# Kernel tuning notes

Hardware: AMD Instinct MI355X
Metric: run time of the kernel (lower is better)

The kernel has to match this reference:

```python
import jax, jax.numpy as jnp
import numpy as np

N_NODES = 50000


def setup_inputs() -> dict:
    key = jax.random.key(0)
    ks = jax.random.split(key, 16)
    f = lambda k, shape: jax.random.normal(k, shape, dtype=jnp.float32) * 0.05
    ri = lambda k, shape: jax.random.randint(k, shape, 0, N_NODES, dtype=jnp.int32)
    return {
        "x": jax.random.normal(ks[0], (N_NODES, 128), dtype=jnp.float32),
        "W1": f(ks[1], (4, 128, 128)),
        "b1": f(ks[2], (4, 128)),
        "W2": f(ks[3], (4, 128, 128)),
        "b2": f(ks[4], (4, 128)),
        "P1w": f(ks[5], (128, 128)),
        "P1b": f(ks[6], (128,)),
        "P2w": f(ks[7], (128, 2)),
        "P2b": f(ks[8], (2,)),
        "src": ri(ks[9], (4, 200000)),
        "dst": ri(ks[10], (4, 200000)),
        "pos_src": ri(ks[11], (4, 200000)),
        "pos_dst": ri(ks[12], (4, 200000)),
        "neg_src": ri(ks[13], (4, 200000)),
        "neg_dst": ri(ks[14], (4, 200000)),
    }


def _hetero_conv(h, src, dst, W, b):
    """One HeteroGraphConv layer: per-relation GraphConv(norm='right'), no activation.

    h: [N, F_in]; src/dst: [R, E]; W: [R, F_in, F_out]; b: [R, F_out].
    Returns per-relation outputs [R, N, F_out] (caller applies activation then sums).
    """
    # sum of source features into destination nodes, per relation
    agg = jax.vmap(lambda s, d: jax.ops.segment_sum(h[s], d, num_segments=N_NODES))(src, dst)  # [R,N,Fin]
    deg = jax.vmap(lambda d: jax.ops.segment_sum(jnp.ones(d.shape, jnp.float32), d, num_segments=N_NODES))(dst)  # [R,N]
    norm = jnp.where(deg > 0, 1.0 / jnp.maximum(deg, 1.0), 0.0)[..., None]  # norm='right': 1/in_degree
    return jnp.einsum("rnf,rfo->rno", agg * norm, W) + b[:, None, :]


def _edge_scores(h, e_src, e_dst, P1w, P1b, P2w, P2b):
    # h[src]*h[dst] -> Linear -> ReLU -> Linear -> softmax -> class-1 prob
    e = h[e_src] * h[e_dst]  # [R,E,F]
    z = jax.nn.relu(jnp.einsum("ref,fo->reo", e, P1w) + P1b)
    logits = jnp.einsum("reo,oc->rec", z, P2w) + P2b
    return jax.nn.softmax(logits, axis=-1)[..., 1]  # [R,E]


def reference(x, W1, b1, W2, b2, P1w, P1b, P2w, P2b,
              src, dst, pos_src, pos_dst, neg_src, neg_dst):
    # Layer 1: relu per relation conv, then HeteroGraphConv sum across relations
    h = jnp.sum(jax.nn.relu(_hetero_conv(x, src, dst, W1, b1)), axis=0)  # [N, hidden]
    # Layer 2: no activation, sum across relations
    h = jnp.sum(_hetero_conv(h, src, dst, W2, b2), axis=0)  # [N, out]
    pos = _edge_scores(h, pos_src, pos_dst, P1w, P1b, P2w, P2b)
    neg = _edge_scores(h, neg_src, neg_dst, P1w, P1b, P2w, P2b)
    return (pos, neg)
```

## Files before the change

kernel.cpp:

```cpp
#include <hip/hip_runtime.h>
#include <hip/hip_bf16.h>
#include <math.h>

#define N_NODES 50000
#define N_EDGES 200000
#define N_REL   4
#define FDIM    128
#define SCAN_BLKS 49

typedef __attribute__((ext_vector_type(8))) short short8;
typedef __attribute__((ext_vector_type(4))) float f32x4;

static __device__ __forceinline__ ushort f2bf(float f) {
  union { float f; unsigned u; } v; v.f = f;
  unsigned r = v.u + 0x7fff + ((v.u >> 16) & 1);
  return (ushort)(r >> 16);
}
static __device__ __forceinline__ unsigned pk2(float lo, float hi) {
  __hip_bfloat162 t = __float22bfloat162_rn(make_float2(lo, hi));
  union { __hip_bfloat162 b; unsigned u; } v; v.b = t;
  return v.u;
}
static __device__ __forceinline__ float lo2f(unsigned u) {
  union { unsigned u; float f; } v; v.u = u << 16; return v.f;
}
static __device__ __forceinline__ float hi2f(unsigned u) {
  union { unsigned u; float f; } v; v.u = u & 0xffff0000u; return v.f;
}

__global__ void cnt_kernel(const int* __restrict__ dst, int* __restrict__ cnt) {
  int i = blockIdx.x * 256 + threadIdx.x;
  if (i < N_REL * N_EDGES) {
    int r = i / N_EDGES;
    atomicAdd(&cnt[r * N_NODES + dst[i]], 1);
  }
}

__global__ __launch_bounds__(1024) void scanA_kernel(
    const int* __restrict__ cnt, int* __restrict__ rowp,
    float* __restrict__ nrm, int* __restrict__ bsum) {
  int r = blockIdx.y, bx = blockIdx.x, t = threadIdx.x;
  int n = bx * 1024 + t;
  int g = r * N_NODES + n;
  int c = 0;
  if (n < N_NODES) {
    c = cnt[g];
    nrm[g] = c > 0 ? 1.f / (float)c : 0.f;
  }
  __shared__ int ts[1024];
  ts[t] = c;
  __syncthreads();
  for (int off = 1; off < 1024; off <<= 1) {
    int v = 0;
    if (t >= off) v = ts[t - off];
    __syncthreads();
    ts[t] += v;
    __syncthreads();
  }
  if (n < N_NODES) rowp[g] = ts[t] - c;
  if (t == 1023) bsum[r * SCAN_BLKS + bx] = ts[t];
}

__global__ void scanB_kernel(int* __restrict__ bsum) {
  int r = threadIdx.x;
  if (r < N_REL) {
    int run = r * N_EDGES;
    for (int b = 0; b < SCAN_BLKS; ++b) {
      int t = bsum[r * SCAN_BLKS + b];
      bsum[r * SCAN_BLKS + b] = run;
      run += t;
    }
  }
}

__global__ void scanC_kernel(int* __restrict__ rowp, int* __restrict__ cursor,
                             const int* __restrict__ bsum) {
  int i = blockIdx.x * 256 + threadIdx.x;
  if (i < N_REL * N_NODES) {
    int r = i / N_NODES;
    int n = i - r * N_NODES;
    int v = rowp[i] + bsum[r * SCAN_BLKS + (n >> 10)];
    rowp[i] = v;
    cursor[i] = v;
  }
}

__global__ void fill_kernel(const int* __restrict__ src, const int* __restrict__ dst,
                            int* __restrict__ cursor, int* __restrict__ csr_s) {
  int i = blockIdx.x * 256 + threadIdx.x;
  if (i < N_REL * N_EDGES) {
    int r = i / N_EDGES;
    int pos = atomicAdd(&cursor[r * N_NODES + dst[i]], 1);
    csr_s[pos] = src[i];
  }
}

__global__ void prep_all_kernel(const float* __restrict__ x, ushort* __restrict__ xb,
                                const float* __restrict__ P1w, ushort* __restrict__ bT,
                                const float* __restrict__ W1, ushort* __restrict__ wT1,
                                const float* __restrict__ W2, ushort* __restrict__ wT2) {
  const int NC = N_NODES * FDIM / 4;
  int i = blockIdx.x * 256 + threadIdx.x;
  if (i < NC) {
    float4 v = ((const float4*)x)[i];
    ((uint2*)xb)[i] = make_uint2(pk2(v.x, v.y), pk2(v.z, v.w));
    return;
  }
  int i2 = i - NC;
  if (i2 < FDIM * FDIM) {
    int c = i2 >> 7, k = i2 & 127;
    bT[i2] = f2bf(P1w[k * FDIM + c]);
    return;
  }
  i2 -= FDIM * FDIM;
  if (i2 < N_REL * FDIM * FDIM) {
    int r = i2 >> 14, c = (i2 >> 7) & 127, k = i2 & 127;
    wT1[i2] = f2bf(W1[(r << 14) + (k << 7) + c]);
    return;
  }
  i2 -= N_REL * FDIM * FDIM;
  if (i2 < N_REL * FDIM * FDIM) {
    int r = i2 >> 14, c = (i2 >> 7) & 127, k = i2 & 127;
    wT2[i2] = f2bf(W2[(r << 14) + (k << 7) + c]);
  }
}

__global__ __launch_bounds__(256) void conv_part_kernel(
    const ushort* __restrict__ hin, const int* __restrict__ rowp,
    const int* __restrict__ cnt, const float* __restrict__ nrm,
    const int* __restrict__ csr_s, const ushort* __restrict__ wT,
    const float* __restrict__ bias, ushort* __restrict__ hpart, int do_relu) {
  __shared__ __align__(16) short elds[64 * 128];
  __shared__ float nrm_lds[64];
  int tid  = threadIdx.x;
  int wave = tid >> 6, lane = tid & 63;
  int base = blockIdx.x * 64;
  int r    = blockIdx.y;
  int ig = tid >> 4, l16 = tid & 15;

  if (tid < 64) {
    int n = base + tid;
    nrm_lds[tid] = (n < N_NODES) ? nrm[r * N_NODES + n] : 0.f;
  }

  for (int rr = ig; rr < 64; rr += 16) {
    int n = base + rr;
    float a8[8];
#pragma unroll
    for (int q = 0; q < 8; ++q) a8[q] = 0.f;
    if (n < N_NODES) {
      int idx = r * N_NODES + n;
      int beg = rowp[idx], num = cnt[idx];
      int j = 0;
      for (; j + 4 <= num; j += 4) {
        int s0 = csr_s[beg + j], s1 = csr_s[beg + j + 1];
        int s2 = csr_s[beg + j + 2], s3 = csr_s[beg + j + 3];
        uint4 v0 = *(const uint4*)(hin + (size_t)s0 * FDIM + l16 * 8);
        uint4 v1 = *(const uint4*)(hin + (size_t)s1 * FDIM + l16 * 8);
        uint4 v2 = *(const uint4*)(hin + (size_t)s2 * FDIM + l16 * 8);
        uint4 v3 = *(const uint4*)(hin + (size_t)s3 * FDIM + l16 * 8);
        a8[0] += lo2f(v0.x) + lo2f(v1.x) + lo2f(v2.x) + lo2f(v3.x);
        a8[1] += hi2f(v0.x) + hi2f(v1.x) + hi2f(v2.x) + hi2f(v3.x);
        a8[2] += lo2f(v0.y) + lo2f(v1.y) + lo2f(v2.y) + lo2f(v3.y);
        a8[3] += hi2f(v0.y) + hi2f(v1.y) + hi2f(v2.y) + hi2f(v3.y);
        a8[4] += lo2f(v0.z) + lo2f(v1.z) + lo2f(v2.z) + lo2f(v3.z);
        a8[5] += hi2f(v0.z) + hi2f(v1.z) + hi2f(v2.z) + hi2f(v3.z);
        a8[6] += lo2f(v0.w) + lo2f(v1.w) + lo2f(v2.w) + lo2f(v3.w);
        a8[7] += hi2f(v0.w) + hi2f(v1.w) + hi2f(v2.w) + hi2f(v3.w);
      }
      for (; j < num; ++j) {
        int s = csr_s[beg + j];
        uint4 v = *(const uint4*)(hin + (size_t)s * FDIM + l16 * 8);
        a8[0] += lo2f(v.x); a8[1] += hi2f(v.x);
        a8[2] += lo2f(v.y); a8[3] += hi2f(v.y);
        a8[4] += lo2f(v.z); a8[5] += hi2f(v.z);
        a8[6] += lo2f(v.w); a8[7] += hi2f(v.w);
      }
    }
    int byte = rr * 256 + l16 * 16;
    byte ^= (rr & 7) << 4;
    *(uint4*)((char*)elds + byte) =
        make_uint4(pk2(a8[0], a8[1]), pk2(a8[2], a8[3]),
                   pk2(a8[4], a8[5]), pk2(a8[6], a8[7]));
  }
  __syncthreads();

  short8 bfrag[2][4];
#pragma unroll
  for (int t2 = 0; t2 < 2; ++t2) {
    int c = wave * 32 + t2 * 16 + (lane & 15);
#pragma unroll
    for (int k0 = 0; k0 < 4; ++k0)
      bfrag[t2][k0] = *(const short8*)(wT + ((size_t)r * FDIM + c) * FDIM + k0 * 32 + (lane >> 4) * 8);
  }

  ushort* hp = hpart + (size_t)r * N_NODES * FDIM;
#pragma unroll
  for (int tr = 0; tr < 4; ++tr) {
    int arow = tr * 16 + (lane & 15);
    short8 afrag[4];
#pragma unroll
    for (int k0 = 0; k0 < 4; ++k0) {
      int byte = arow * 256 + k0 * 64 + (lane >> 4) * 16;
      byte ^= (arow & 7) << 4;
      afrag[k0] = *(const short8*)((const char*)elds + byte);
    }
#pragma unroll
    for (int t2 = 0; t2 < 2; ++t2) {
      f32x4 acc = {0.f, 0.f, 0.f, 0.f};
#pragma unroll
      for (int k0 = 0; k0 < 4; ++k0)
        acc = __builtin_amdgcn_mfma_f32_16x16x32_bf16(afrag[k0], bfrag[t2][k0], acc, 0, 0, 0);
      int col = wave * 32 + t2 * 16 + (lane & 15);
      float bv = bias[r * FDIM + col];
#pragma unroll
      for (int j2 = 0; j2 < 4; ++j2) {
        int n = base + tr * 16 + (lane >> 4) * 4 + j2;
        if (n < N_NODES) {
          float nr = nrm_lds[tr * 16 + (lane >> 4) * 4 + j2];
          float v = acc[j2] * nr + bv;
          if (do_relu) v = fmaxf(v, 0.f);
          hp[(size_t)n * FDIM + col] = f2bf(v);
        }
      }
    }
  }
}

__global__ void finalize_kernel(const ushort* __restrict__ hpart, ushort* __restrict__ hout) {
  int i = blockIdx.x * 256 + threadIdx.x;
  const int NV = N_NODES * FDIM / 8;
  if (i < NV) {
    uint4 a = ((const uint4*)hpart)[i];
    uint4 b = ((const uint4*)(hpart + (size_t)N_NODES * FDIM))[i];
    uint4 c = ((const uint4*)(hpart + (size_t)2 * N_NODES * FDIM))[i];
    uint4 d = ((const uint4*)(hpart + (size_t)3 * N_NODES * FDIM))[i];
    float s0 = lo2f(a.x) + lo2f(b.x) + lo2f(c.x) + lo2f(d.x);
    float s1 = hi2f(a.x) + hi2f(b.x) + hi2f(c.x) + hi2f(d.x);
    float s2 = lo2f(a.y) + lo2f(b.y) + lo2f(c.y) + lo2f(d.y);
    float s3 = hi2f(a.y) + hi2f(b.y) + hi2f(c.y) + hi2f(d.y);
    float s4 = lo2f(a.z) + lo2f(b.z) + lo2f(c.z) + lo2f(d.z);
    float s5 = hi2f(a.z) + hi2f(b.z) + hi2f(c.z) + hi2f(d.z);
    float s6 = lo2f(a.w) + lo2f(b.w) + lo2f(c.w) + lo2f(d.w);
    float s7 = hi2f(a.w) + hi2f(b.w) + hi2f(c.w) + hi2f(d.w);
    ((uint4*)hout)[i] = make_uint4(pk2(s0, s1), pk2(s2, s3), pk2(s4, s5), pk2(s6, s7));
  }
}

__global__ __launch_bounds__(256) void edge_mfma_kernel(
    const ushort* __restrict__ hb,
    const int* __restrict__ psrc, const int* __restrict__ pdst,
    const int* __restrict__ nsrc, const int* __restrict__ ndst,
    const ushort* __restrict__ bT, const float* __restrict__ P1b,
    const float* __restrict__ P2w, const float* __restrict__ P2b,
    float* __restrict__ out) {
  __shared__ __align__(16) short elds[64 * 128];
  __shared__ float partials[4][64];

  int tid  = threadIdx.x;
  int wave = tid >> 6, lane = tid & 63;
  int b = blockIdx.x;
  const int *esrc, *edst;
  float* o;
  int base;
  if (b < (N_REL * N_EDGES) / 64) {
    esrc = psrc; edst = pdst; o = out; base = b * 64;
  } else {
    esrc = nsrc; edst = ndst; o = out + (size_t)N_REL * N_EDGES;
    base = (b - (N_REL * N_EDGES) / 64) * 64;
  }

  int c0 = (2 * wave) * 16 + (lane & 15);
  int c1 = c0 + 16;
  float bz0 = P1b[c0], bz1 = P1b[c1];
  float wd0 = P2w[c0 * 2 + 1] - P2w[c0 * 2];
  float wd1 = P2w[c1 * 2 + 1] - P2w[c1 * 2];
  float cdiff = P2b[1] - P2b[0];

  short8 bfrag[2][4];
#pragma unroll
  for (int t2 = 0; t2 < 2; ++t2) {
    int c = (2 * wave + t2) * 16 + (lane & 15);
#pragma unroll
    for (int k0 = 0; k0 < 4; ++k0)
      bfrag[t2][k0] = *(const short8*)(bT + (size_t)c * 128 + k0 * 32 + (lane >> 4) * 8);
  }

  uint4 av[4], gv[4];
#pragma unroll
  for (int j = 0; j < 4; ++j) {
    int flat = j * 256 + tid;
    int row = flat >> 4, f8 = flat & 15;
    int ge = base + row;
    int s = esrc[ge], d = edst[ge];
    av[j] = *(const uint4*)(hb + (size_t)s * FDIM + f8 * 8);
    gv[j] = *(const uint4*)(hb + (size_t)d * FDIM + f8 * 8);
  }
#pragma unroll
  for (int j = 0; j < 4; ++j) {
    int flat = j * 256 + tid;
    int row = flat >> 4, f8 = flat & 15;
    unsigned w0 = pk2(lo2f(av[j].x) * lo2f(gv[j].x), hi2f(av[j].x) * hi2f(gv[j].x));
    unsigned w1 = pk2(lo2f(av[j].y) * lo2f(gv[j].y), hi2f(av[j].y) * hi2f(gv[j].y));
    unsigned w2 = pk2(lo2f(av[j].z) * lo2f(gv[j].z), hi2f(av[j].z) * hi2f(gv[j].z));
    unsigned w3 = pk2(lo2f(av[j].w) * lo2f(gv[j].w), hi2f(av[j].w) * hi2f(gv[j].w));
    int byte = row * 256 + f8 * 16;
    byte ^= (row & 7) << 4;
    *(uint4*)((char*)elds + byte) = make_uint4(w0, w1, w2, w3);
  }
  __syncthreads();

  float part[4][4];
#pragma unroll
  for (int tr = 0; tr < 4; ++tr)
#pragma unroll
    for (int j2 = 0; j2 < 4; ++j2) part[tr][j2] = 0.f;

#pragma unroll
  for (int tr = 0; tr < 4; ++tr) {
    int arow = tr * 16 + (lane & 15);
    short8 afrag[4];
#pragma unroll
    for (int k0 = 0; k0 < 4; ++k0) {
      int byte = arow * 256 + k0 * 64 + (lane >> 4) * 16;
      byte ^= (arow & 7) << 4;
      afrag[k0] = *(const short8*)((const char*)elds + byte);
    }
#pragma unroll
    for (int t2 = 0; t2 < 2; ++t2) {
      f32x4 acc = {0.f, 0.f, 0.f, 0.f};
#pragma unroll
      for (int k0 = 0; k0 < 4; ++k0)
        acc = __builtin_amdgcn_mfma_f32_16x16x32_bf16(afrag[k0], bfrag[t2][k0], acc, 0, 0, 0);
      float bz = t2 ? bz1 : bz0;
      float wdv = t2 ? wd1 : wd0;
#pragma unroll
      for (int j2 = 0; j2 < 4; ++j2)
        part[tr][j2] += fmaxf(acc[j2] + bz, 0.f) * wdv;
    }
  }

#pragma unroll
  for (int tr = 0; tr < 4; ++tr)
#pragma unroll
    for (int j2 = 0; j2 < 4; ++j2) {
      float v = part[tr][j2];
      v += __shfl_xor(v, 1);
      v += __shfl_xor(v, 2);
      v += __shfl_xor(v, 4);
      v += __shfl_xor(v, 8);
      if ((lane & 15) == 0) partials[wave][tr * 16 + (lane >> 4) * 4 + j2] = v;
    }
  __syncthreads();

  if (tid < 64) {
    float s2 = partials[0][tid] + partials[1][tid] + partials[2][tid] + partials[3][tid] + cdiff;
    o[base + tid] = 1.f / (1.f + expf(-s2));
  }
}

extern "C" void kernel_launch(void* const* d_in, const int* in_sizes, int n_in,
                              void* d_out, int out_size, void* d_ws, size_t ws_size,
                              hipStream_t stream) {
  const float* x   = (const float*)d_in[0];
  const float* W1  = (const float*)d_in[1];
  const float* b1  = (const float*)d_in[2];
  const float* W2  = (const float*)d_in[3];
  const float* b2  = (const float*)d_in[4];
  const float* P1w = (const float*)d_in[5];
  const float* P1b = (const float*)d_in[6];
  const float* P2w = (const float*)d_in[7];
  const float* P2b = (const float*)d_in[8];
  const int* src     = (const int*)d_in[9];
  const int* dst     = (const int*)d_in[10];
  const int* pos_src = (const int*)d_in[11];
  const int* pos_dst = (const int*)d_in[12];
  const int* neg_src = (const int*)d_in[13];
  const int* neg_dst = (const int*)d_in[14];
  float* out = (float*)d_out;

  char* ws = (char*)d_ws;
  int*    cnt    = (int*)ws;     ws += (size_t)N_REL * N_NODES * 4;
  int*    rowp   = (int*)ws;     ws += (size_t)N_REL * N_NODES * 4;
  int*    cursor = (int*)ws;     ws += (size_t)N_REL * N_NODES * 4;
  int*    csr_s  = (int*)ws;     ws += (size_t)N_REL * N_EDGES * 4;
  float*  nrm    = (float*)ws;   ws += (size_t)N_REL * N_NODES * 4;
  int*    bsum   = (int*)ws;     ws += 4096;
  ushort* bT     = (ushort*)ws;  ws += (size_t)FDIM * FDIM * 2;
  ushort* wT1    = (ushort*)ws;  ws += (size_t)N_REL * FDIM * FDIM * 2;
  ushort* wT2    = (ushort*)ws;  ws += (size_t)N_REL * FDIM * FDIM * 2;
  ushort* xb     = (ushort*)ws;  ws += (size_t)N_NODES * FDIM * 2;
  ushort* h1b    = (ushort*)ws;  ws += (size_t)N_NODES * FDIM * 2;
  ushort* h2b    = (ushort*)ws;  ws += (size_t)N_NODES * FDIM * 2;
  ushort* hacc   = (ushort*)ws;

  hipMemsetAsync(cnt, 0, (size_t)N_REL * N_NODES * 4, stream);
  cnt_kernel<<<(N_REL * N_EDGES + 255) / 256, 256, 0, stream>>>(dst, cnt);
  scanA_kernel<<<dim3(SCAN_BLKS, N_REL), 1024, 0, stream>>>(cnt, rowp, nrm, bsum);
  scanB_kernel<<<1, 64, 0, stream>>>(bsum);
  scanC_kernel<<<(N_REL * N_NODES + 255) / 256, 256, 0, stream>>>(rowp, cursor, bsum);
  fill_kernel<<<(N_REL * N_EDGES + 255) / 256, 256, 0, stream>>>(src, dst, cursor, csr_s);
  {
    int total = N_NODES * FDIM / 4 + FDIM * FDIM + 2 * N_REL * FDIM * FDIM;
    prep_all_kernel<<<(total + 255) / 256, 256, 0, stream>>>(x, xb, P1w, bT, W1, wT1, W2, wT2);
  }

  conv_part_kernel<<<dim3((N_NODES + 63) / 64, N_REL), 256, 0, stream>>>(
      xb, rowp, cnt, nrm, csr_s, wT1, b1, hacc, 1);
  finalize_kernel<<<(N_NODES * FDIM / 8 + 255) / 256, 256, 0, stream>>>(hacc, h1b);
  conv_part_kernel<<<dim3((N_NODES + 63) / 64, N_REL), 256, 0, stream>>>(
      h1b, rowp, cnt, nrm, csr_s, wT2, b2, hacc, 0);
  finalize_kernel<<<(N_NODES * FDIM / 8 + 255) / 256, 256, 0, stream>>>(hacc, h2b);

  edge_mfma_kernel<<<2 * (N_REL * N_EDGES) / 64, 256, 0, stream>>>(
      h2b, pos_src, pos_dst, neg_src, neg_dst, bT, P1b, P2w, P2b, out);
}
```

Before: 492.3 us.

## Process two 64-edge tiles per block with second tile's gathers issued early

Each edge-scoring block now handles 128 edges instead of 64. The gathers for both tiles are issued up front, so the second tile's global loads are in flight while the first tile is multiplied and run through the MFMAs. This halves the block count and amortizes the per-block weight-fragment loads. In exchange each thread holds more registers for the extra gathered vectors and accumulators, which may lower occupancy.

```diff
diff --git a/kernel.cpp b/kernel.cpp
--- a/kernel.cpp
+++ b/kernel.cpp
@@ -255,19 +255,20 @@
     const float* __restrict__ P2w, const float* __restrict__ P2b,
     float* __restrict__ out) {
   __shared__ __align__(16) short elds[64 * 128];
-  __shared__ float partials[4][64];
+  __shared__ float partials[4][128];
 
   int tid  = threadIdx.x;
   int wave = tid >> 6, lane = tid & 63;
   int b = blockIdx.x;
+  const int HALF = (N_REL * N_EDGES) / 128;
   const int *esrc, *edst;
   float* o;
   int base;
-  if (b < (N_REL * N_EDGES) / 64) {
-    esrc = psrc; edst = pdst; o = out; base = b * 64;
+  if (b < HALF) {
+    esrc = psrc; edst = pdst; o = out; base = b * 128;
   } else {
     esrc = nsrc; edst = ndst; o = out + (size_t)N_REL * N_EDGES;
-    base = (b - (N_REL * N_EDGES) / 64) * 64;
+    base = (b - HALF) * 128;
   }
 
   int c0 = (2 * wave) * 16 + (lane & 15);
@@ -286,35 +287,45 @@
       bfrag[t2][k0] = *(const short8*)(bT + (size_t)c * 128 + k0 * 32 + (lane >> 4) * 8);
   }
 
-  uint4 av[4], gv[4];
+  uint4 av0[4], gv0[4], av1[4], gv1[4];
 #pragma unroll
   for (int j = 0; j < 4; ++j) {
     int flat = j * 256 + tid;
     int row = flat >> 4, f8 = flat & 15;
     int ge = base + row;
     int s = esrc[ge], d = edst[ge];
-    av[j] = *(const uint4*)(hb + (size_t)s * FDIM + f8 * 8);
-    gv[j] = *(const uint4*)(hb + (size_t)d * FDIM + f8 * 8);
+    av0[j] = *(const uint4*)(hb + (size_t)s * FDIM + f8 * 8);
+    gv0[j] = *(const uint4*)(hb + (size_t)d * FDIM + f8 * 8);
   }
 #pragma unroll
   for (int j = 0; j < 4; ++j) {
     int flat = j * 256 + tid;
     int row = flat >> 4, f8 = flat & 15;
-    unsigned w0 = pk2(lo2f(av[j].x) * lo2f(gv[j].x), hi2f(av[j].x) * hi2f(gv[j].x));
-    unsigned w1 = pk2(lo2f(av[j].y) * lo2f(gv[j].y), hi2f(av[j].y) * hi2f(gv[j].y));
-    unsigned w2 = pk2(lo2f(av[j].z) * lo2f(gv[j].z), hi2f(av[j].z) * hi2f(gv[j].z));
-    unsigned w3 = pk2(lo2f(av[j].w) * lo2f(gv[j].w), hi2f(av[j].w) * hi2f(gv[j].w));
+    int ge = base + 64 + row;
+    int s = esrc[ge], d = edst[ge];
+    av1[j] = *(const uint4*)(hb + (size_t)s * FDIM + f8 * 8);
+    gv1[j] = *(const uint4*)(hb + (size_t)d * FDIM + f8 * 8);
+  }
+
+  float part0[4][4], part1[4][4];
+#pragma unroll
+  for (int tr = 0; tr < 4; ++tr)
+#pragma unroll
+    for (int j2 = 0; j2 < 4; ++j2) { part0[tr][j2] = 0.f; part1[tr][j2] = 0.f; }
+
+#pragma unroll
+  for (int j = 0; j < 4; ++j) {
+    int flat = j * 256 + tid;
+    int row = flat >> 4, f8 = flat & 15;
+    unsigned w0 = pk2(lo2f(av0[j].x) * lo2f(gv0[j].x), hi2f(av0[j].x) * hi2f(gv0[j].x));
+    unsigned w1 = pk2(lo2f(av0[j].y) * lo2f(gv0[j].y), hi2f(av0[j].y) * hi2f(gv0[j].y));
+    unsigned w2 = pk2(lo2f(av0[j].z) * lo2f(gv0[j].z), hi2f(av0[j].z) * hi2f(gv0[j].z));
+    unsigned w3 = pk2(lo2f(av0[j].w) * lo2f(gv0[j].w), hi2f(av0[j].w) * hi2f(gv0[j].w));
     int byte = row * 256 + f8 * 16;
     byte ^= (row & 7) << 4;
     *(uint4*)((char*)elds + byte) = make_uint4(w0, w1, w2, w3);
   }
   __syncthreads();
-
-  float part[4][4];
-#pragma unroll
-  for (int tr = 0; tr < 4; ++tr)
-#pragma unroll
-    for (int j2 = 0; j2 < 4; ++j2) part[tr][j2] = 0.f;
 
 #pragma unroll
   for (int tr = 0; tr < 4; ++tr) {
@@ -336,7 +347,46 @@
       float wdv = t2 ? wd1 : wd0;
 #pragma unroll
       for (int j2 = 0; j2 < 4; ++j2)
-        part[tr][j2] += fmaxf(acc[j2] + bz, 0.f) * wdv;
+        part0[tr][j2] += fmaxf(acc[j2] + bz, 0.f) * wdv;
+    }
+  }
+  __syncthreads();
+
+#pragma unroll
+  for (int j = 0; j < 4; ++j) {
+    int flat = j * 256 + tid;
+    int row = flat >> 4, f8 = flat & 15;
+    unsigned w0 = pk2(lo2f(av1[j].x) * lo2f(gv1[j].x), hi2f(av1[j].x) * hi2f(gv1[j].x));
+    unsigned w1 = pk2(lo2f(av1[j].y) * lo2f(gv1[j].y), hi2f(av1[j].y) * hi2f(gv1[j].y));
+    unsigned w2 = pk2(lo2f(av1[j].z) * lo2f(gv1[j].z), hi2f(av1[j].z) * hi2f(gv1[j].z));
+    unsigned w3 = pk2(lo2f(av1[j].w) * lo2f(gv1[j].w), hi2f(av1[j].w) * hi2f(gv1[j].w));
+    int byte = row * 256 + f8 * 16;
+    byte ^= (row & 7) << 4;
+    *(uint4*)((char*)elds + byte) = make_uint4(w0, w1, w2, w3);
+  }
+  __syncthreads();
+
+#pragma unroll
+  for (int tr = 0; tr < 4; ++tr) {
+    int arow = tr * 16 + (lane & 15);
+    short8 afrag[4];
+#pragma unroll
+    for (int k0 = 0; k0 < 4; ++k0) {
+      int byte = arow * 256 + k0 * 64 + (lane >> 4) * 16;
+      byte ^= (arow & 7) << 4;
+      afrag[k0] = *(const short8*)((const char*)elds + byte);
+    }
+#pragma unroll
+    for (int t2 = 0; t2 < 2; ++t2) {
+      f32x4 acc = {0.f, 0.f, 0.f, 0.f};
+#pragma unroll
+      for (int k0 = 0; k0 < 4; ++k0)
+        acc = __builtin_amdgcn_mfma_f32_16x16x32_bf16(afrag[k0], bfrag[t2][k0], acc, 0, 0, 0);
+      float bz = t2 ? bz1 : bz0;
+      float wdv = t2 ? wd1 : wd0;
+#pragma unroll
+      for (int j2 = 0; j2 < 4; ++j2)
+        part1[tr][j2] += fmaxf(acc[j2] + bz, 0.f) * wdv;
     }
   }
 
@@ -344,16 +394,25 @@
   for (int tr = 0; tr < 4; ++tr)
 #pragma unroll
     for (int j2 = 0; j2 < 4; ++j2) {
-      float v = part[tr][j2];
+      float v = part0[tr][j2];
       v += __shfl_xor(v, 1);
       v += __shfl_xor(v, 2);
       v += __shfl_xor(v, 4);
       v += __shfl_xor(v, 8);
-      if ((lane & 15) == 0) partials[wave][tr * 16 + (lane >> 4) * 4 + j2] = v;
-    }
-  __syncthreads();
-
-  if (tid < 64) {
+      float u = part1[tr][j2];
+      u += __shfl_xor(u, 1);
+      u += __shfl_xor(u, 2);
+      u += __shfl_xor(u, 4);
+      u += __shfl_xor(u, 8);
+      if ((lane & 15) == 0) {
+        int rowi = tr * 16 + (lane >> 4) * 4 + j2;
+        partials[wave][rowi] = v;
+        partials[wave][64 + rowi] = u;
+      }
+    }
+  __syncthreads();
+
+  if (tid < 128) {
     float s2 = partials[0][tid] + partials[1][tid] + partials[2][tid] + partials[3][tid] + cdiff;
     o[base + tid] = 1.f / (1.f + expf(-s2));
   }
@@ -412,6 +471,6 @@
       h1b, rowp, cnt, nrm, csr_s, wT2, b2, hacc, 0);
   finalize_kernel<<<(N_NODES * FDIM / 8 + 255) / 256, 256, 0, stream>>>(hacc, h2b);
 
-  edge_mfma_kernel<<<2 * (N_REL * N_EDGES) / 64, 256, 0, stream>>>(
+  edge_mfma_kernel<<<2 * (N_REL * N_EDGES) / 128, 256, 0, stream>>>(
       h2b, pos_src, pos_dst, neg_src, neg_dst, bT, P1b, P2w, P2b, out);
 }
```

Measured after the change: 464.6 us. 5.6% less time.
